# Kernel tuning notes

Measured on AMD Instinct MI355X. Metric: run time of the kernel, lower is better.

The kernel has to match this reference:

```python
import jax, jax.numpy as jnp
import numpy as np

K_SIZE = 7  # kernel_size (odd)


def setup_inputs() -> dict:
    key = jax.random.key(0)
    k0, k1, k2, k3 = jax.random.split(key, 4)
    B, C, H, W = 4, 128, 192, 192
    O, K = 128, K_SIZE
    x = jax.random.normal(k0, (B, C, H, W), dtype=jnp.float32)
    offsets = jax.random.normal(k1, (B, K, H, W), dtype=jnp.float32) * 0.5
    tumor_center = jax.random.uniform(k2, (B, 2), dtype=jnp.float32) * H  # (h, w) coords
    kernel_w = jax.random.normal(k3, (O * K, C), dtype=jnp.float32) / np.sqrt(C)  # 1x1 conv weight
    kernel_b = jnp.zeros((O * K,), dtype=jnp.float32)
    return {"x": x, "offsets": offsets, "tumor_center": tumor_center,
            "kernel_w": kernel_w, "kernel_b": kernel_b}


def reference(x, offsets, tumor_center, kernel_w, kernel_b):
    B, C, H, W = x.shape
    K = K_SIZE
    O = kernel_w.shape[0] // K
    pad = K // 2
    dt = x.dtype

    # ---- radial flow grid (faithful to source; see note below) ----
    h_c = tumor_center[:, 0][:, None, None]          # [B,1,1]
    w_c = tumor_center[:, 1][:, None, None]
    h_idx = jnp.arange(H, dtype=dt)[None, :, None]   # [1,H,1]
    w_idx = jnp.arange(W, dtype=dt)[None, None, :]   # [1,1,W]
    dh = h_idx - h_c                                  # [B,H,W]
    dw = w_idx - w_c
    rnorm = jnp.sqrt(dh * dh + dw * dw + 1e-6)
    dir_h = dh / rnorm
    dir_w = dw / rnorm
    base = jnp.linspace(-pad, pad, K, dtype=dt).reshape(1, K, 1, 1)
    h_grid = base * dir_h[:, None] + offsets          # [B,K,H,W]
    w_grid = base * dir_w[:, None] + offsets
    h_grid = h_grid / (H - 1) * 2
    w_grid = w_grid / (W - 1) * 2
    grid = jnp.stack([w_grid, h_grid], axis=-1)       # [B,K,H,W,2]
    # grid_sample is applied to x reshaped to [B*H*W, C, 1, 1] (a single-pixel
    # input) with align_corners=True: the unnormalize factor (size-1)=0 pins the
    # sample location to pixel (0,0) for ANY grid value, so
    # sampled[bhw, c, k] == x[bhw, c] exactly (grid has zero influence/grad).
    del grid

    # ---- dynamic per-pixel kernels via 1x1 conv ----
    kern = jnp.einsum('bchw,fc->bfhw', x, kernel_w) + kernel_b[None, :, None, None]
    kern = kern.reshape(B, O, K, H, W)

    # ---- bmm([BHW,C,K], [BHW,K,O]) then sum over C, fused into one einsum ----
    out = jnp.einsum('bchw,bokhw->bohw', x, kern)     # [B,O,H,W]
    return out
```

## Files before the change

### kernel.cpp

```cpp
#include <hip/hip_runtime.h>
#include <hip/hip_bf16.h>

#define BB   4
#define CC   128
#define HH   192
#define WWd  192
#define HWp  (HH*WWd)
#define OO   128
#define KK   7
#define NPIX (BB*HWp)
#define TILE 64
#define BUF_BYTES 17408

typedef short bf16x8 __attribute__((ext_vector_type(8)));
typedef float f32x4  __attribute__((ext_vector_type(4)));

static __device__ __forceinline__ unsigned f2bf(float f) {
    union { __hip_bfloat16 h; unsigned short u; } cvt;
    cvt.h = __float2bfloat16(f);
    return (unsigned)cvt.u;
}

__global__ __launch_bounds__(256) void prep_kernel(const float* __restrict__ kw,
                                                   const float* __restrict__ kb,
                                                   unsigned short* __restrict__ wfrag,
                                                   float* __restrict__ bsum) {
    int tid = blockIdx.x * 256 + threadIdx.x;
    int o = tid >> 7, c = tid & 127;
    float s = 0.f;
#pragma unroll
    for (int k = 0; k < KK; ++k) s += kw[(o*KK + k)*CC + c];
    int wv = o >> 5, mt = (o >> 4) & 1, lo = o & 15;
    int ks = c >> 5, g = (c >> 3) & 3, j = c & 7;
    int idx = ((((wv*2 + mt)*4 + ks)*64) + (lo + 16*g))*8 + j;
    wfrag[idx] = (unsigned short)f2bf(s);
    if (c == 0) {
        float bs = 0.f;
#pragma unroll
        for (int k = 0; k < KK; ++k) bs += kb[o*KK + k];
        bsum[o] = bs;
    }
}

__global__ __launch_bounds__(256, 8) void conv_kernel(const float* __restrict__ x,
                                                      const unsigned short* __restrict__ wfrag,
                                                      const float* __restrict__ bsum,
                                                      float* __restrict__ out) {
    __shared__ __align__(16) unsigned char buf[BUF_BYTES];
    __shared__ float sPart[4][TILE];

    const int t = threadIdx.x;
    const int w = t >> 6;
    const int l = t & 63;
    const int lo16 = l & 15, g4 = l >> 4;

    const int pixBase = blockIdx.x * TILE;
    const int bIdx   = pixBase / HWp;
    const int hwBase = pixBase - bIdx * HWp;
    const float* xb  = x + (size_t)bIdx * CC * HWp + hwBase;

    {
        const int p4 = lo16 * 4;
        float pa = 0.f, pb = 0.f, pc = 0.f, pd = 0.f;
#pragma unroll
        for (int it = 0; it < 8; ++it) {
            const int c = it*16 + w*4 + g4;
            const float4 v = *reinterpret_cast<const float4*>(xb + (size_t)c * HWp + p4);
            pa += v.x; pb += v.y; pc += v.z; pd += v.w;
            uint2 u;
            u.x = f2bf(v.x) | (f2bf(v.y) << 16);
            u.y = f2bf(v.z) | (f2bf(v.w) << 16);
            *reinterpret_cast<uint2*>(&buf[c*128 + p4*2]) = u;
        }
        pa += __shfl_xor(pa, 16); pa += __shfl_xor(pa, 32);
        pb += __shfl_xor(pb, 16); pb += __shfl_xor(pb, 32);
        pc += __shfl_xor(pc, 16); pc += __shfl_xor(pc, 32);
        pd += __shfl_xor(pd, 16); pd += __shfl_xor(pd, 32);
        if (l < 16)
            *reinterpret_cast<float4*>(&sPart[w][p4]) = make_float4(pa, pb, pc, pd);
    }
    __syncthreads();

    unsigned pk[16];
    {
        const int p2 = l * 2;
#pragma unroll
        for (int i = 0; i < 4; ++i)
#pragma unroll
            for (int h = 0; h < 4; ++h) {
                const int c = w*32 + i*8 + h*2;
                const unsigned e0 = *reinterpret_cast<const unsigned short*>(&buf[c*128 + p2]);
                const unsigned e1 = *reinterpret_cast<const unsigned short*>(&buf[(c+1)*128 + p2]);
                pk[i*4 + h] = e0 | (e1 << 16);
            }
    }
    __syncthreads();

#pragma unroll
    for (int i = 0; i < 4; ++i) {
        uint4 q4 = make_uint4(pk[i*4+0], pk[i*4+1], pk[i*4+2], pk[i*4+3]);
        *reinterpret_cast<uint4*>(&buf[l*272 + w*64 + i*16]) = q4;
    }
    __syncthreads();

    f32x4 acc[2][4];
#pragma unroll
    for (int mt = 0; mt < 2; ++mt)
#pragma unroll
        for (int nt = 0; nt < 4; ++nt)
            acc[mt][nt] = (f32x4){0.f, 0.f, 0.f, 0.f};

    const unsigned short* wf = wfrag + (size_t)w * 2*4*64*8;
    for (int ks = 0; ks < 4; ++ks) {
        const bf16x8 a0 = *reinterpret_cast<const bf16x8*>(wf + ((size_t)(0*4 + ks)*64 + l)*8);
        const bf16x8 a1 = *reinterpret_cast<const bf16x8*>(wf + ((size_t)(1*4 + ks)*64 + l)*8);
        bf16x8 bfr[4];
#pragma unroll
        for (int nt = 0; nt < 4; ++nt)
            bfr[nt] = *reinterpret_cast<const bf16x8*>(&buf[(nt*16 + lo16)*272 + ks*64 + g4*16]);
#pragma unroll
        for (int nt = 0; nt < 4; ++nt) {
            acc[0][nt] = __builtin_amdgcn_mfma_f32_16x16x32_bf16(a0, bfr[nt], acc[0][nt], 0, 0, 0);
            acc[1][nt] = __builtin_amdgcn_mfma_f32_16x16x32_bf16(a1, bfr[nt], acc[1][nt], 0, 0, 0);
        }
    }

    float* ob = out + (size_t)bIdx * OO * HWp + hwBase + lo16;
#pragma unroll
    for (int nt = 0; nt < 4; ++nt) {
        const int pp = nt*16 + lo16;
        const float sv = sPart[0][pp] + sPart[1][pp] + sPart[2][pp] + sPart[3][pp];
#pragma unroll
        for (int mt = 0; mt < 2; ++mt) {
            const int o0 = w*32 + mt*16 + g4*4;
            const float4 bs4 = *reinterpret_cast<const float4*>(bsum + o0);
#pragma unroll
            for (int r = 0; r < 4; ++r) {
                const float bsv = (r == 0) ? bs4.x : (r == 1) ? bs4.y : (r == 2) ? bs4.z : bs4.w;
                ob[(size_t)(o0 + r) * HWp + nt*16] = (acc[mt][nt][r] + bsv) * sv;
            }
        }
    }
}

extern "C" void kernel_launch(void* const* d_in, const int* in_sizes, int n_in,
                              void* d_out, int out_size, void* d_ws, size_t ws_size,
                              hipStream_t stream) {
    const float* x  = (const float*)d_in[0];
    const float* kw = (const float*)d_in[3];
    const float* kb = (const float*)d_in[4];
    float* outp = (float*)d_out;

    unsigned short* wfrag = (unsigned short*)d_ws;
    float* bsum = (float*)((char*)d_ws + 32768);

    prep_kernel<<<dim3(64), dim3(256), 0, stream>>>(kw, kb, wfrag, bsum);
    conv_kernel<<<dim3(NPIX / TILE), dim3(256), 0, stream>>>(x, wfrag, bsum, outp);
}
```

Measured before the change: 35.32 us.

## Load x per-pixel per-lane to write transposed tile directly, preload weight fragments

```diff
diff --git a/kernel.cpp b/kernel.cpp
--- a/kernel.cpp
+++ b/kernel.cpp
@@ -10,7 +10,7 @@
 #define KK   7
 #define NPIX (BB*HWp)
 #define TILE 64
-#define BUF_BYTES 17408
+#define XT_PITCH_B 272
 
 typedef short bf16x8 __attribute__((ext_vector_type(8)));
 typedef float f32x4  __attribute__((ext_vector_type(4)));
@@ -42,11 +42,11 @@
     }
 }
 
-__global__ __launch_bounds__(256, 8) void conv_kernel(const float* __restrict__ x,
+__global__ __launch_bounds__(256, 4) void conv_kernel(const float* __restrict__ x,
                                                       const unsigned short* __restrict__ wfrag,
                                                       const float* __restrict__ bsum,
                                                       float* __restrict__ out) {
-    __shared__ __align__(16) unsigned char buf[BUF_BYTES];
+    __shared__ __align__(16) unsigned char xTb[TILE * XT_PITCH_B];
     __shared__ float sPart[4][TILE];
 
     const int t = threadIdx.x;
@@ -57,49 +57,34 @@
     const int pixBase = blockIdx.x * TILE;
     const int bIdx   = pixBase / HWp;
     const int hwBase = pixBase - bIdx * HWp;
-    const float* xb  = x + (size_t)bIdx * CC * HWp + hwBase;
+    const float* xb  = x + (size_t)bIdx * CC * HWp + hwBase + l;
 
-    {
-        const int p4 = lo16 * 4;
-        float pa = 0.f, pb = 0.f, pc = 0.f, pd = 0.f;
+    bf16x8 afrag[2][4];
+    const unsigned short* wf = wfrag + (size_t)w * 2*4*64*8;
 #pragma unroll
-        for (int it = 0; it < 8; ++it) {
-            const int c = it*16 + w*4 + g4;
-            const float4 v = *reinterpret_cast<const float4*>(xb + (size_t)c * HWp + p4);
-            pa += v.x; pb += v.y; pc += v.z; pd += v.w;
-            uint2 u;
-            u.x = f2bf(v.x) | (f2bf(v.y) << 16);
-            u.y = f2bf(v.z) | (f2bf(v.w) << 16);
-            *reinterpret_cast<uint2*>(&buf[c*128 + p4*2]) = u;
-        }
-        pa += __shfl_xor(pa, 16); pa += __shfl_xor(pa, 32);
-        pb += __shfl_xor(pb, 16); pb += __shfl_xor(pb, 32);
-        pc += __shfl_xor(pc, 16); pc += __shfl_xor(pc, 32);
-        pd += __shfl_xor(pd, 16); pd += __shfl_xor(pd, 32);
-        if (l < 16)
-            *reinterpret_cast<float4*>(&sPart[w][p4]) = make_float4(pa, pb, pc, pd);
+    for (int mt = 0; mt < 2; ++mt)
+#pragma unroll
+        for (int ks = 0; ks < 4; ++ks)
+            afrag[mt][ks] = *reinterpret_cast<const bf16x8*>(wf + ((size_t)(mt*4 + ks)*64 + l)*8);
+
+    float v[32];
+#pragma unroll
+    for (int i = 0; i < 8; ++i) {
+        const int c0 = w*32 + i*4;
+#pragma unroll
+        for (int j = 0; j < 4; ++j)
+            v[i*4 + j] = xb[(size_t)(c0 + j) * HWp];
     }
-    __syncthreads();
-
-    unsigned pk[16];
-    {
-        const int p2 = l * 2;
+    float csum = 0.f;
 #pragma unroll
-        for (int i = 0; i < 4; ++i)
+    for (int i = 0; i < 32; ++i) csum += v[i];
+    sPart[w][l] = csum;
 #pragma unroll
-            for (int h = 0; h < 4; ++h) {
-                const int c = w*32 + i*8 + h*2;
-                const unsigned e0 = *reinterpret_cast<const unsigned short*>(&buf[c*128 + p2]);
-                const unsigned e1 = *reinterpret_cast<const unsigned short*>(&buf[(c+1)*128 + p2]);
-                pk[i*4 + h] = e0 | (e1 << 16);
-            }
-    }
-    __syncthreads();
-
-#pragma unroll
-    for (int i = 0; i < 4; ++i) {
-        uint4 q4 = make_uint4(pk[i*4+0], pk[i*4+1], pk[i*4+2], pk[i*4+3]);
-        *reinterpret_cast<uint4*>(&buf[l*272 + w*64 + i*16]) = q4;
+    for (int i = 0; i < 8; ++i) {
+        uint2 u;
+        u.x = f2bf(v[i*4+0]) | (f2bf(v[i*4+1]) << 16);
+        u.y = f2bf(v[i*4+2]) | (f2bf(v[i*4+3]) << 16);
+        *reinterpret_cast<uint2*>(&xTb[l*XT_PITCH_B + (w*32 + i*4)*2]) = u;
     }
     __syncthreads();
 
@@ -110,18 +95,16 @@
         for (int nt = 0; nt < 4; ++nt)
             acc[mt][nt] = (f32x4){0.f, 0.f, 0.f, 0.f};
 
-    const unsigned short* wf = wfrag + (size_t)w * 2*4*64*8;
     for (int ks = 0; ks < 4; ++ks) {
-        const bf16x8 a0 = *reinterpret_cast<const bf16x8*>(wf + ((size_t)(0*4 + ks)*64 + l)*8);
-        const bf16x8 a1 = *reinterpret_cast<const bf16x8*>(wf + ((size_t)(1*4 + ks)*64 + l)*8);
         bf16x8 bfr[4];
 #pragma unroll
         for (int nt = 0; nt < 4; ++nt)
-            bfr[nt] = *reinterpret_cast<const bf16x8*>(&buf[(nt*16 + lo16)*272 + ks*64 + g4*16]);
+            bfr[nt] = *reinterpret_cast<const bf16x8*>(
+                &xTb[(nt*16 + lo16)*XT_PITCH_B + ks*64 + g4*16]);
 #pragma unroll
         for (int nt = 0; nt < 4; ++nt) {
-            acc[0][nt] = __builtin_amdgcn_mfma_f32_16x16x32_bf16(a0, bfr[nt], acc[0][nt], 0, 0, 0);
-            acc[1][nt] = __builtin_amdgcn_mfma_f32_16x16x32_bf16(a1, bfr[nt], acc[1][nt], 0, 0, 0);
+            acc[0][nt] = __builtin_amdgcn_mfma_f32_16x16x32_bf16(afrag[0][ks], bfr[nt], acc[0][nt], 0, 0, 0);
+            acc[1][nt] = __builtin_amdgcn_mfma_f32_16x16x32_bf16(afrag[1][ks], bfr[nt], acc[1][nt], 0, 0, 0);
         }
     }
 
```

After: 33.73 us. 4.5% less time.
